# Performance work log

Measured on AMD Instinct MI355X. Metric: run time of the kernel, lower is better.

Reference implementation:

```python
import jax, jax.numpy as jnp
import numpy as np

IN_DIM = 1024
OUT_DIM = 1024
QK_DIM = OUT_DIM // 4  # 256


def setup_inputs() -> dict:
    key = jax.random.key(0)
    kx, ky, kq, kk, kv = jax.random.split(key, 5)
    B, Sq, Sk = 16, 2048, 2048
    x = jax.random.normal(kx, (B, Sq, IN_DIM), dtype=jnp.float32)
    y = jax.random.normal(ky, (B, Sk, IN_DIM), dtype=jnp.float32)
    s = 1.0 / np.sqrt(IN_DIM)
    Wq = jax.random.normal(kq, (IN_DIM, QK_DIM), dtype=jnp.float32) * s
    Wk = jax.random.normal(kk, (IN_DIM, QK_DIM), dtype=jnp.float32) * s
    Wv = jax.random.normal(kv, (IN_DIM, OUT_DIM), dtype=jnp.float32) * s
    return {"x": x, "y": y, "Wq": Wq, "Wk": Wk, "Wv": Wv}


def reference(x, y, Wq, Wk, Wv):
    # q: [B,Sq,dk], k: [B,Sk,dk]
    q = jnp.einsum("bsd,dk->bsk", x, Wq)
    k = jnp.einsum("btd,dk->btk", y, Wk)
    # NOTE: original scales by out_dim**0.5, not qk dim
    scores = jnp.einsum("bsk,btk->bst", q, k) / jnp.sqrt(jnp.float32(OUT_DIM))
    attn = jax.nn.softmax(scores, axis=-1)
    v = jnp.einsum("btd,de->bte", y, Wv)
    out = jnp.einsum("bst,bte->bse", attn, v)
    return out + x
```

## Files before the change

kernel.cpp:

```cpp
#include <hip/hip_runtime.h>

typedef __attribute__((ext_vector_type(8))) short bf16x8;
typedef __attribute__((ext_vector_type(4))) short s16x4;
typedef __attribute__((ext_vector_type(4))) float f32x4;

#define MFMA16(a,b,c) __builtin_amdgcn_mfma_f32_16x16x32_bf16((a),(b),(c),0,0,0)

__device__ __forceinline__ unsigned short f2bf(float f) {
  unsigned int u = __float_as_uint(f);
  return (unsigned short)((u + 0x7fffu + ((u >> 16) & 1u)) >> 16);
}
__device__ __forceinline__ float bf2f(unsigned short u) {
  return __uint_as_float(((unsigned int)u) << 16);
}

__device__ __forceinline__ void gload16(const void* g, void* l) {
  __builtin_amdgcn_global_load_lds((const __attribute__((address_space(1))) void*)g,
                                   (__attribute__((address_space(3))) void*)l, 16, 0, 0);
}

__global__ __launch_bounds__(256) void cvt_bf16(const float* __restrict__ in,
                                                unsigned short* __restrict__ out, int n8) {
  for (int i = blockIdx.x * 256 + threadIdx.x; i < n8; i += gridDim.x * 256) {
    float4 a = ((const float4*)in)[2 * i];
    float4 b = ((const float4*)in)[2 * i + 1];
    s16x4 p0, p1;
    p0[0] = f2bf(a.x); p0[1] = f2bf(a.y); p0[2] = f2bf(a.z); p0[3] = f2bf(a.w);
    p1[0] = f2bf(b.x); p1[1] = f2bf(b.y); p1[2] = f2bf(b.z); p1[3] = f2bf(b.w);
    ((s16x4*)out)[2 * i] = p0;
    ((s16x4*)out)[2 * i + 1] = p1;
  }
}

__global__ __launch_bounds__(256) void tcvt(const float* __restrict__ W,
                                            unsigned short* __restrict__ Wt, int K, int N) {
  __shared__ float t[32][33];
  const int n0 = blockIdx.x * 32, k0 = blockIdx.y * 32;
  const int c = threadIdx.x & 31, r8 = threadIdx.x >> 5;
#pragma unroll
  for (int p = 0; p < 4; ++p) {
    int r = r8 + p * 8;
    t[r][c] = W[(size_t)(k0 + r) * N + n0 + c];
  }
  __syncthreads();
#pragma unroll
  for (int p = 0; p < 4; ++p) {
    int r = r8 + p * 8;
    Wt[(size_t)(n0 + r) * K + k0 + c] = f2bf(t[c][r]);
  }
}

__global__ __launch_bounds__(256) void proj_gemm(
    const unsigned short* __restrict__ A, const unsigned short* __restrict__ Bt,
    void* __restrict__ Cv, int N, int mode, float scale)
{
  __shared__ __align__(16) unsigned short As[2][4096];
  __shared__ __align__(16) unsigned short Bs[2][4096];
  const int tid = threadIdx.x, lane = tid & 63, w = tid >> 6;
  const int wr = w >> 1, wc = w & 1;
  const int lrow = lane & 15, lg = lane >> 4;
  const size_t bm = (size_t)blockIdx.x * 128;
  const size_t bn = (size_t)blockIdx.y * 128;
  const int rl = lane >> 2, cq = lane & 3;

  auto stage = [&](int kt, int buf) {
#pragma unroll
    for (int u = 0; u < 2; ++u) {
      int row = w * 32 + u * 16 + rl;
      gload16(A  + (bm + row) * 1024 + kt * 32 + cq * 8, &As[buf][(w * 32 + u * 16) * 32]);
      gload16(Bt + (bn + row) * 1024 + kt * 32 + cq * 8, &Bs[buf][(w * 32 + u * 16) * 32]);
    }
  };

  f32x4 acc[4][4] = {};
  stage(0, 0);
  __syncthreads();

  for (int kt = 0; kt < 32; ++kt) {
    const int cur = kt & 1;
    if (kt + 1 < 32) stage(kt + 1, cur ^ 1);
    bf16x8 af[4], bfr[4];
#pragma unroll
    for (int i = 0; i < 4; ++i)
      af[i] = *(const bf16x8*)&As[cur][(wr * 64 + i * 16 + lrow) * 32 + lg * 8];
#pragma unroll
    for (int j = 0; j < 4; ++j)
      bfr[j] = *(const bf16x8*)&Bs[cur][(wc * 64 + j * 16 + lrow) * 32 + lg * 8];
    __builtin_amdgcn_s_setprio(1);
#pragma unroll
    for (int i = 0; i < 4; ++i)
#pragma unroll
      for (int j = 0; j < 4; ++j)
        acc[i][j] = MFMA16(af[i], bfr[j], acc[i][j]);
    __builtin_amdgcn_s_setprio(0);
    __syncthreads();
  }

  const int orow0 = blockIdx.x * 128 + wr * 64;
  const int ocol0 = blockIdx.y * 128 + wc * 64;
  if (mode == 0) {
    unsigned short* C = (unsigned short*)Cv;
#pragma unroll
    for (int i = 0; i < 4; ++i)
#pragma unroll
      for (int j = 0; j < 4; ++j) {
        int col = ocol0 + j * 16 + lrow;
#pragma unroll
        for (int r = 0; r < 4; ++r) {
          int row = orow0 + i * 16 + lg * 4 + r;
          C[(size_t)row * N + col] = f2bf(acc[i][j][r] * scale);
        }
      }
  } else {
    unsigned char* C8 = (unsigned char*)Cv;
#pragma unroll
    for (int i = 0; i < 4; ++i) {
      int m0 = orow0 + i * 16 + lg * 4;
      int bb = m0 >> 11, t = m0 & 2047;
#pragma unroll
      for (int j = 0; j < 4; ++j) {
        int e = ocol0 + j * 16 + lrow;
        int pk = 0;
        pk = __builtin_amdgcn_cvt_pk_fp8_f32(acc[i][j][0], acc[i][j][1], pk, false);
        pk = __builtin_amdgcn_cvt_pk_fp8_f32(acc[i][j][2], acc[i][j][3], pk, true);
        *(unsigned int*)(C8 + (size_t)bb * 2097152 + (size_t)e * 2048 + t) = (unsigned int)pk;
      }
    }
  }
}

#define SBAR  do { __builtin_amdgcn_s_barrier(); __builtin_amdgcn_sched_barrier(0); } while (0)

template<int NT, int NTIL, int MODE>
__global__ __launch_bounds__(512) void gemm4p(
    const unsigned short* __restrict__ Aall, const unsigned short* __restrict__ Ball,
    size_t abatch, size_t bbatch, int lda, int ldb,
    unsigned short* __restrict__ Cb, const float* __restrict__ X,
    float* __restrict__ Out, int b0, int nb)
{
  __shared__ __align__(16) unsigned short lds[65536];
  const int bid = blockIdx.x;
  const int bloc = bid % nb, tl = bid / nb;
  const int mtile = tl / NTIL, ntile = tl % NTIL;
  const int gb = b0 + bloc;
  const unsigned short* Ag = Aall + (MODE == 0 ? (size_t)gb : (size_t)bloc) * abatch
                                  + (size_t)mtile * 256 * lda;
  const unsigned short* Bg = Ball + (size_t)gb * bbatch + (size_t)ntile * 256 * ldb;

  const int tid = threadIdx.x, lane = tid & 63, w = tid >> 6;
  const int wm = w >> 2, wn = w & 3;
  const int lrow = lane & 15, lg = lane >> 4;
  char* lb = (char*)lds;

  auto stageU = [&](const unsigned short* G, int ld, int kofs, int ubyte) {
#pragma unroll
    for (int i = 0; i < 2; ++i) {
      int c = tid + 512 * i;
      int row = c >> 2, q = c & 3;
      int qs = q ^ ((row >> 1) & 3);
      gload16(G + (size_t)row * ld + kofs + qs * 8, lb + ubyte + c * 16);
    }
  };
  auto rdfrag = [&](int ubyte, int row) -> bf16x8 {
    return *(const bf16x8*)(lb + ubyte + row * 64 + ((lg ^ ((row >> 1) & 3)) << 4));
  };

  f32x4 acc[8][4] = {};
  bf16x8 afA[4], afB[4], bfrA[4], bfrB[4];

  stageU(Ag, lda, 0,  (0 * 2 + 0) * 16384);
  stageU(Bg, ldb, 0,  (1 * 2 + 0) * 16384);
  stageU(Ag, lda, 32, (2 * 2 + 0) * 16384);
  stageU(Bg, ldb, 32, (3 * 2 + 0) * 16384);
  stageU(Ag, lda, 64, (0 * 2 + 1) * 16384);
  stageU(Bg, ldb, 64, (1 * 2 + 1) * 16384);
  asm volatile("s_waitcnt vmcnt(8)" ::: "memory");
  SBAR;
#pragma unroll
  for (int i = 0; i < 4; ++i) afA[i] = rdfrag(0, wm * 128 + i * 16 + lrow);
#pragma unroll
  for (int nf = 0; nf < 4; ++nf) bfrA[nf] = rdfrag(2 * 16384, wn * 64 + nf * 16 + lrow);

  for (int T = 0; T < NT; ++T) {
    const int pc = T & 1, pn = (T + 1) & 1;
    const int a1b = (2 * 2 + pc) * 16384, b1b = (3 * 2 + pc) * 16384;
    const int a0b = (0 * 2 + pc) * 16384, b0b = (1 * 2 + pc) * 16384;
    const int t1 = (T + 1 < NT) ? T + 1 : 0;
    const int t2 = (T + 2 < NT) ? T + 2 : 0;

#pragma unroll
    for (int i = 0; i < 4; ++i) afB[i] = rdfrag(a0b, wm * 128 + (i + 4) * 16 + lrow);
    stageU(Ag, lda, t1 * 64 + 32, (2 * 2 + pn) * 16384);
    asm volatile("s_waitcnt lgkmcnt(4)" ::: "memory");
    __builtin_amdgcn_sched_barrier(0);
    __builtin_amdgcn_s_setprio(1);
#pragma unroll
    for (int mf = 0; mf < 4; ++mf)
#pragma unroll
      for (int nf = 0; nf < 4; ++nf)
        acc[mf][nf] = MFMA16(afA[mf], bfrA[nf], acc[mf][nf]);
    __builtin_amdgcn_s_setprio(0);
    asm volatile("s_waitcnt vmcnt(6)" ::: "memory");
    SBAR;

#pragma unroll
    for (int i = 0; i < 4; ++i) afA[i] = rdfrag(a1b, wm * 128 + i * 16 + lrow);
#pragma unroll
    for (int nf = 0; nf < 4; ++nf) bfrB[nf] = rdfrag(b1b, wn * 64 + nf * 16 + lrow);
    stageU(Bg, ldb, t1 * 64 + 32, (3 * 2 + pn) * 16384);
    asm volatile("s_waitcnt lgkmcnt(8)" ::: "memory");
    __builtin_amdgcn_sched_barrier(0);
    __builtin_amdgcn_s_setprio(1);
#pragma unroll
    for (int mf = 0; mf < 4; ++mf)
#pragma unroll
      for (int nf = 0; nf < 4; ++nf)
        acc[mf + 4][nf] = MFMA16(afB[mf], bfrA[nf], acc[mf + 4][nf]);
    __builtin_amdgcn_s_setprio(0);
    SBAR;

#pragma unroll
    for (int i = 0; i < 4; ++i) afB[i] = rdfrag(a1b, wm * 128 + (i + 4) * 16 + lrow);
    stageU(Ag, lda, t2 * 64, (0 * 2 + pc) * 16384);
    asm volatile("s_waitcnt lgkmcnt(4)" ::: "memory");
    __builtin_amdgcn_sched_barrier(0);
    __builtin_amdgcn_s_setprio(1);
#pragma unroll
    for (int mf = 0; mf < 4; ++mf)
#pragma unroll
      for (int nf = 0; nf < 4; ++nf)
        acc[mf][nf] = MFMA16(afA[mf], bfrB[nf], acc[mf][nf]);
    __builtin_amdgcn_s_setprio(0);
    asm volatile("s_waitcnt vmcnt(6)" ::: "memory");
    SBAR;

#pragma unroll
    for (int i = 0; i < 4; ++i) afA[i] = rdfrag((0 * 2 + pn) * 16384, wm * 128 + i * 16 + lrow);
#pragma unroll
    for (int nf = 0; nf < 4; ++nf) bfrA[nf] = rdfrag((1 * 2 + pn) * 16384, wn * 64 + nf * 16 + lrow);
    stageU(Bg, ldb, t2 * 64, (1 * 2 + pc) * 16384);
    asm volatile("s_waitcnt lgkmcnt(8)" ::: "memory");
    __builtin_amdgcn_sched_barrier(0);
    __builtin_amdgcn_s_setprio(1);
#pragma unroll
    for (int mf = 0; mf < 4; ++mf)
#pragma unroll
      for (int nf = 0; nf < 4; ++nf)
        acc[mf + 4][nf] = MFMA16(afB[mf], bfrB[nf], acc[mf + 4][nf]);
    __builtin_amdgcn_s_setprio(0);
    SBAR;
  }

  {
    unsigned short* Cp = Cb + (size_t)bloc * 2048 * 2048;
#pragma unroll
    for (int mf = 0; mf < 8; ++mf)
#pragma unroll
      for (int r = 0; r < 4; ++r) {
        int row = mtile * 256 + wm * 128 + mf * 16 + lg * 4 + r;
#pragma unroll
        for (int nf = 0; nf < 4; ++nf) {
          int col = ntile * 256 + wn * 64 + nf * 16 + lrow;
          Cp[(size_t)row * 2048 + col] = f2bf(acc[mf][nf][r]);
        }
      }
  }
  (void)X; (void)Out;
}

__global__ __launch_bounds__(256) void softmax_kernel(
    const unsigned short* __restrict__ Sp, unsigned char* __restrict__ Pp) {
  const int row = blockIdx.x * 4 + (threadIdx.x >> 6);
  const int lane = threadIdx.x & 63;
  const unsigned short* rp = Sp + (size_t)row * 2048;
  bf16x8 raw[4];
#pragma unroll
  for (int c = 0; c < 4; ++c) raw[c] = *(const bf16x8*)(rp + c * 512 + lane * 8);
  float v[32];
#pragma unroll
  for (int c = 0; c < 4; ++c)
#pragma unroll
    for (int j = 0; j < 8; ++j) v[c * 8 + j] = bf2f((unsigned short)raw[c][j]);
  float mx = v[0];
#pragma unroll
  for (int j = 1; j < 32; ++j) mx = fmaxf(mx, v[j]);
  mx = fmaxf(mx, __shfl_xor(mx, 1));
  mx = fmaxf(mx, __shfl_xor(mx, 2));
  mx = fmaxf(mx, __shfl_xor(mx, 4));
  mx = fmaxf(mx, __shfl_xor(mx, 8));
  mx = fmaxf(mx, __shfl_xor(mx, 16));
  mx = fmaxf(mx, __shfl_xor(mx, 32));
  float sum = 0.f;
#pragma unroll
  for (int j = 0; j < 32; ++j) { v[j] = __expf(v[j] - mx); sum += v[j]; }
  sum += __shfl_xor(sum, 1);
  sum += __shfl_xor(sum, 2);
  sum += __shfl_xor(sum, 4);
  sum += __shfl_xor(sum, 8);
  sum += __shfl_xor(sum, 16);
  sum += __shfl_xor(sum, 32);
  const float scale = 64.0f / sum;
  unsigned char* rp8 = Pp + (size_t)row * 2048;
#pragma unroll
  for (int c = 0; c < 4; ++c) {
    int lo = 0, hi = 0;
    lo = __builtin_amdgcn_cvt_pk_fp8_f32(v[c * 8 + 0] * scale, v[c * 8 + 1] * scale, lo, false);
    lo = __builtin_amdgcn_cvt_pk_fp8_f32(v[c * 8 + 2] * scale, v[c * 8 + 3] * scale, lo, true);
    hi = __builtin_amdgcn_cvt_pk_fp8_f32(v[c * 8 + 4] * scale, v[c * 8 + 5] * scale, hi, false);
    hi = __builtin_amdgcn_cvt_pk_fp8_f32(v[c * 8 + 6] * scale, v[c * 8 + 7] * scale, hi, true);
    uint2 o; o.x = (unsigned int)lo; o.y = (unsigned int)hi;
    *(uint2*)(rp8 + c * 512 + lane * 8) = o;
  }
}

__global__ __launch_bounds__(512) void pvf8_kernel(
    const unsigned char* __restrict__ Pp,
    const unsigned char* __restrict__ Vt,
    const float* __restrict__ X, float* __restrict__ Out,
    int b0, int nb)
{
  __shared__ __align__(16) unsigned char lds[4][32768];
  const int bloc = blockIdx.x % nb, tl = blockIdx.x / nb;
  const int mtile = tl >> 2, ntile = tl & 3;
  const int gb = b0 + bloc;
  const unsigned char* Ag = Pp + (size_t)bloc * 4194304 + (size_t)mtile * 256 * 2048;
  const unsigned char* Bg = Vt + (size_t)gb * 2097152 + (size_t)ntile * 256 * 2048;
  const int NT = 32;
  const int tid = threadIdx.x, lane = tid & 63, w = tid >> 6;
  const int wm = w >> 2, wn = w & 3;
  const int lrow = lane & 15, lg = lane >> 4;

  auto stageT = [&](int jt, int slot) {
#pragma unroll
    for (int i = 0; i < 2; ++i) {
      int c = tid + 512 * i; int row = c >> 2; int q = (c & 3) ^ ((row >> 1) & 3);
      gload16(Ag + (size_t)row * 2048 + jt * 64 + q * 16, &lds[slot][c * 16]);
    }
#pragma unroll
    for (int i = 0; i < 2; ++i) {
      int c = tid + 512 * i; int row = c >> 2; int q = (c & 3) ^ ((row >> 1) & 3);
      gload16(Bg + (size_t)row * 2048 + jt * 64 + q * 16, &lds[slot][16384 + c * 16]);
    }
  };

  f32x4 acc[8][4] = {};
  stageT(0, 0); stageT(1, 1); stageT(2, 2);

  for (int jt = 0; jt < NT; ++jt) {
    if (jt < NT - 2)       asm volatile("s_waitcnt vmcnt(8)" ::: "memory");
    else if (jt == NT - 2) asm volatile("s_waitcnt vmcnt(4)" ::: "memory");
    else                   asm volatile("s_waitcnt vmcnt(0)" ::: "memory");
    __builtin_amdgcn_sched_barrier(0);
    __builtin_amdgcn_s_barrier();
    __builtin_amdgcn_sched_barrier(0);
    if (jt + 3 < NT) stageT(jt + 3, (jt + 3) & 3);
    const int slot = jt & 3;
    long2 av[8], bv[4];
#pragma unroll
    for (int mf = 0; mf < 8; ++mf) {
      int row = wm * 128 + mf * 16 + lrow;
      av[mf] = *(const long2*)&lds[slot][row * 64 + ((lg ^ ((row >> 1) & 3)) << 4)];
    }
#pragma unroll
    for (int nf = 0; nf < 4; ++nf) {
      int row = wn * 64 + nf * 16 + lrow;
      bv[nf] = *(const long2*)&lds[slot][16384 + row * 64 + ((lg ^ ((row >> 1) & 3)) << 4)];
    }
    __builtin_amdgcn_s_setprio(1);
#pragma unroll
    for (int mf = 0; mf < 8; ++mf)
#pragma unroll
      for (int nf = 0; nf < 4; ++nf) {
        acc[mf][nf] = __builtin_amdgcn_mfma_f32_16x16x32_fp8_fp8(av[mf].x, bv[nf].x, acc[mf][nf], 0, 0, 0);
        acc[mf][nf] = __builtin_amdgcn_mfma_f32_16x16x32_fp8_fp8(av[mf].y, bv[nf].y, acc[mf][nf], 0, 0, 0);
      }
    __builtin_amdgcn_s_setprio(0);
  }

#pragma unroll
  for (int mf = 0; mf < 8; ++mf)
#pragma unroll
    for (int r = 0; r < 4; ++r) {
      int row = mtile * 256 + wm * 128 + mf * 16 + lg * 4 + r;
      const float* xr = X   + ((size_t)gb * 2048 + row) * 1024;
      float*      orp = Out + ((size_t)gb * 2048 + row) * 1024;
#pragma unroll
      for (int nf = 0; nf < 4; ++nf) {
        int col = ntile * 256 + wn * 64 + nf * 16 + lrow;
        orp[col] = acc[mf][nf][r] * 0.015625f + xr[col];
      }
    }
}

extern "C" void kernel_launch(void* const* d_in, const int* in_sizes, int n_in,
                              void* d_out, int out_size, void* d_ws, size_t ws_size,
                              hipStream_t stream) {
  (void)in_sizes; (void)n_in; (void)out_size;
  const float* x  = (const float*)d_in[0];
  const float* y  = (const float*)d_in[1];
  const float* Wq = (const float*)d_in[2];
  const float* Wk = (const float*)d_in[3];
  const float* Wv = (const float*)d_in[4];
  float* out = (float*)d_out;

  unsigned short* xb = (unsigned short*)d_out;
  unsigned short* yb = xb + (size_t)16 * 2048 * 1024;

  char* p = (char*)d_ws;
  unsigned short* Wqt = (unsigned short*)p;  p += (size_t)256 * 1024 * 2;
  unsigned short* Wkt = (unsigned short*)p;  p += (size_t)256 * 1024 * 2;
  unsigned short* Wvt = (unsigned short*)p;  p += (size_t)1024 * 1024 * 2;
  unsigned short* qws = (unsigned short*)p;  p += (size_t)16 * 2048 * 256 * 2;
  unsigned short* kws = (unsigned short*)p;  p += (size_t)16 * 2048 * 256 * 2;
  unsigned char*  vt8 = (unsigned char*)p;   p += (size_t)16 * 1024 * 2048;
  char* dyn = p;
  const size_t fixed_bytes = (size_t)(dyn - (char*)d_ws);
  const size_t per_batch = (size_t)2048 * 2048 * 2 + (size_t)2048 * 2048;
  int nb = 1;
  if      (ws_size >= fixed_bytes + 16 * per_batch) nb = 16;
  else if (ws_size >= fixed_bytes + 8  * per_batch) nb = 8;
  else if (ws_size >= fixed_bytes + 4  * per_batch) nb = 4;
  else if (ws_size >= fixed_bytes + 2  * per_batch) nb = 2;
  else nb = 1;
  unsigned short* Sp = (unsigned short*)dyn;
  unsigned char*  Pp = (unsigned char*)(dyn + (size_t)nb * 2048 * 2048 * 2);

  const int n8 = (16 * 2048 * 1024) / 8;
  cvt_bf16<<<2048, 256, 0, stream>>>(x, xb, n8);
  cvt_bf16<<<2048, 256, 0, stream>>>(y, yb, n8);
  tcvt<<<dim3(8, 32),  256, 0, stream>>>(Wq, Wqt, 1024, 256);
  tcvt<<<dim3(8, 32),  256, 0, stream>>>(Wk, Wkt, 1024, 256);
  tcvt<<<dim3(32, 32), 256, 0, stream>>>(Wv, Wvt, 1024, 1024);

  proj_gemm<<<dim3(256, 2), 256, 0, stream>>>(xb, Wqt, (void*)qws, 256, 0, 0.03125f);
  proj_gemm<<<dim3(256, 2), 256, 0, stream>>>(yb, Wkt, (void*)kws, 256, 0, 1.0f);
  proj_gemm<<<dim3(256, 8), 256, 0, stream>>>(yb, Wvt, (void*)vt8, 1024, 2, 1.0f);

  for (int b0 = 0; b0 < 16; b0 += nb) {
    gemm4p<4, 8, 0><<<nb * 64, 512, 0, stream>>>(
        qws, kws, (size_t)2048 * 256, (size_t)2048 * 256, 256, 256,
        Sp, nullptr, nullptr, b0, nb);
    softmax_kernel<<<nb * 512, 256, 0, stream>>>(Sp, Pp);
    pvf8_kernel<<<nb * 32, 512, 0, stream>>>(Pp, vt8, x, out, b0, nb);
  }
}
```

Measured before the change: 510.8 us.

## Pre-pack V into MFMA fragment layout and load B operands directly from global

The V projection epilogue now writes fp8 V in a blocked layout where each 16-column by 64-token group is a contiguous 1 KB fragment. The PV kernel then loads its B fragments straight from global memory into registers instead of staging them through LDS. The output tile is halved to 256x128, which doubles the grid, halves LDS use, and drops the accumulators to 8x2. The intent is less LDS traffic and more occupancy and parallelism, at the cost of unhidden global-load latency on V and more redundant reads of the P tile across blocks.

```diff
diff --git a/kernel.cpp b/kernel.cpp
--- a/kernel.cpp
+++ b/kernel.cpp
@@ -117,13 +117,17 @@
     for (int i = 0; i < 4; ++i) {
       int m0 = orow0 + i * 16 + lg * 4;
       int bb = m0 >> 11, t = m0 & 2047;
+      int tw = t >> 6, t64 = t & 63;
 #pragma unroll
       for (int j = 0; j < 4; ++j) {
         int e = ocol0 + j * 16 + lrow;
+        int eg = e >> 4;
         int pk = 0;
         pk = __builtin_amdgcn_cvt_pk_fp8_f32(acc[i][j][0], acc[i][j][1], pk, false);
         pk = __builtin_amdgcn_cvt_pk_fp8_f32(acc[i][j][2], acc[i][j][3], pk, true);
-        *(unsigned int*)(C8 + (size_t)bb * 2097152 + (size_t)e * 2048 + t) = (unsigned int)pk;
+        *(unsigned int*)(C8 + (size_t)bb * 2097152
+                            + ((size_t)(eg * 32 + tw)) * 1024 + lrow * 64 + t64)
+            = (unsigned int)pk;
       }
     }
   }
@@ -184,7 +188,7 @@
   for (int T = 0; T < NT; ++T) {
     const int pc = T & 1, pn = (T + 1) & 1;
     const int a1b = (2 * 2 + pc) * 16384, b1b = (3 * 2 + pc) * 16384;
-    const int a0b = (0 * 2 + pc) * 16384, b0b = (1 * 2 + pc) * 16384;
+    const int a0b = (0 * 2 + pc) * 16384;
     const int t1 = (T + 1 < NT) ? T + 1 : 0;
     const int t2 = (T + 2 < NT) ? T + 2 : 0;
 
@@ -315,66 +319,78 @@
 
 __global__ __launch_bounds__(512) void pvf8_kernel(
     const unsigned char* __restrict__ Pp,
-    const unsigned char* __restrict__ Vt,
+    const unsigned char* __restrict__ Vp,
     const float* __restrict__ X, float* __restrict__ Out,
     int b0, int nb)
 {
-  __shared__ __align__(16) unsigned char lds[4][32768];
+  __shared__ __align__(16) unsigned char lds[4][16384];
   const int bloc = blockIdx.x % nb, tl = blockIdx.x / nb;
-  const int mtile = tl >> 2, ntile = tl & 3;
+  const int mtile = tl >> 3, ntile = tl & 7;
   const int gb = b0 + bloc;
   const unsigned char* Ag = Pp + (size_t)bloc * 4194304 + (size_t)mtile * 256 * 2048;
-  const unsigned char* Bg = Vt + (size_t)gb * 2097152 + (size_t)ntile * 256 * 2048;
+  const unsigned char* Vb = Vp + (size_t)gb * 2097152;
   const int NT = 32;
   const int tid = threadIdx.x, lane = tid & 63, w = tid >> 6;
   const int wm = w >> 2, wn = w & 3;
   const int lrow = lane & 15, lg = lane >> 4;
 
-  auto stageT = [&](int jt, int slot) {
+  auto stageA = [&](int jt) {
+    unsigned char* dst = lds[jt & 3];
 #pragma unroll
     for (int i = 0; i < 2; ++i) {
       int c = tid + 512 * i; int row = c >> 2; int q = (c & 3) ^ ((row >> 1) & 3);
-      gload16(Ag + (size_t)row * 2048 + jt * 64 + q * 16, &lds[slot][c * 16]);
-    }
-#pragma unroll
-    for (int i = 0; i < 2; ++i) {
-      int c = tid + 512 * i; int row = c >> 2; int q = (c & 3) ^ ((row >> 1) & 3);
-      gload16(Bg + (size_t)row * 2048 + jt * 64 + q * 16, &lds[slot][16384 + c * 16]);
+      gload16(Ag + (size_t)row * 2048 + jt * 64 + q * 16, dst + c * 16);
     }
   };
 
-  f32x4 acc[8][4] = {};
-  stageT(0, 0); stageT(1, 1); stageT(2, 2);
+  f32x4 acc[8][2] = {};
+  stageA(0); stageA(1); stageA(2);
+  asm volatile("s_waitcnt vmcnt(4)" ::: "memory");
 
   for (int jt = 0; jt < NT; ++jt) {
-    if (jt < NT - 2)       asm volatile("s_waitcnt vmcnt(8)" ::: "memory");
-    else if (jt == NT - 2) asm volatile("s_waitcnt vmcnt(4)" ::: "memory");
-    else                   asm volatile("s_waitcnt vmcnt(0)" ::: "memory");
-    __builtin_amdgcn_sched_barrier(0);
     __builtin_amdgcn_s_barrier();
-    __builtin_amdgcn_sched_barrier(0);
-    if (jt + 3 < NT) stageT(jt + 3, (jt + 3) & 3);
-    const int slot = jt & 3;
-    long2 av[8], bv[4];
-#pragma unroll
-    for (int mf = 0; mf < 8; ++mf) {
-      int row = wm * 128 + mf * 16 + lrow;
-      av[mf] = *(const long2*)&lds[slot][row * 64 + ((lg ^ ((row >> 1) & 3)) << 4)];
-    }
-#pragma unroll
-    for (int nf = 0; nf < 4; ++nf) {
-      int row = wn * 64 + nf * 16 + lrow;
-      bv[nf] = *(const long2*)&lds[slot][16384 + row * 64 + ((lg ^ ((row >> 1) & 3)) << 4)];
-    }
-    __builtin_amdgcn_s_setprio(1);
-#pragma unroll
-    for (int mf = 0; mf < 8; ++mf)
-#pragma unroll
-      for (int nf = 0; nf < 4; ++nf) {
-        acc[mf][nf] = __builtin_amdgcn_mfma_f32_16x16x32_fp8_fp8(av[mf].x, bv[nf].x, acc[mf][nf], 0, 0, 0);
-        acc[mf][nf] = __builtin_amdgcn_mfma_f32_16x16x32_fp8_fp8(av[mf].y, bv[nf].y, acc[mf][nf], 0, 0, 0);
-      }
-    __builtin_amdgcn_s_setprio(0);
+    long2 bv[2];
+#pragma unroll
+    for (int nf = 0; nf < 2; ++nf) {
+      int eg = ntile * 8 + wn * 2 + nf;
+      bv[nf] = *(const long2*)(Vb + ((size_t)(eg * 32 + jt)) * 1024 + lrow * 64 + lg * 16);
+    }
+    if (jt + 3 < NT) stageA(jt + 3);
+    const unsigned char* Ab = lds[jt & 3];
+    {
+      long2 av[4];
+#pragma unroll
+      for (int mf = 0; mf < 4; ++mf) {
+        int row = wm * 128 + mf * 16 + lrow;
+        av[mf] = *(const long2*)(Ab + row * 64 + ((lg ^ ((row >> 1) & 3)) << 4));
+      }
+      __builtin_amdgcn_s_setprio(1);
+#pragma unroll
+      for (int mf = 0; mf < 4; ++mf)
+#pragma unroll
+        for (int nf = 0; nf < 2; ++nf) {
+          acc[mf][nf] = __builtin_amdgcn_mfma_f32_16x16x32_fp8_fp8(av[mf].x, bv[nf].x, acc[mf][nf], 0, 0, 0);
+          acc[mf][nf] = __builtin_amdgcn_mfma_f32_16x16x32_fp8_fp8(av[mf].y, bv[nf].y, acc[mf][nf], 0, 0, 0);
+        }
+      __builtin_amdgcn_s_setprio(0);
+    }
+    {
+      long2 av[4];
+#pragma unroll
+      for (int mf = 0; mf < 4; ++mf) {
+        int row = wm * 128 + (mf + 4) * 16 + lrow;
+        av[mf] = *(const long2*)(Ab + row * 64 + ((lg ^ ((row >> 1) & 3)) << 4));
+      }
+      __builtin_amdgcn_s_setprio(1);
+#pragma unroll
+      for (int mf = 0; mf < 4; ++mf)
+#pragma unroll
+        for (int nf = 0; nf < 2; ++nf) {
+          acc[mf + 4][nf] = __builtin_amdgcn_mfma_f32_16x16x32_fp8_fp8(av[mf].x, bv[nf].x, acc[mf + 4][nf], 0, 0, 0);
+          acc[mf + 4][nf] = __builtin_amdgcn_mfma_f32_16x16x32_fp8_fp8(av[mf].y, bv[nf].y, acc[mf + 4][nf], 0, 0, 0);
+        }
+      __builtin_amdgcn_s_setprio(0);
+    }
   }
 
 #pragma unroll
@@ -385,8 +401,8 @@
       const float* xr = X   + ((size_t)gb * 2048 + row) * 1024;
       float*      orp = Out + ((size_t)gb * 2048 + row) * 1024;
 #pragma unroll
-      for (int nf = 0; nf < 4; ++nf) {
-        int col = ntile * 256 + wn * 64 + nf * 16 + lrow;
+      for (int nf = 0; nf < 2; ++nf) {
+        int col = ntile * 128 + wn * 32 + nf * 16 + lrow;
         orp[col] = acc[mf][nf][r] * 0.015625f + xr[col];
       }
     }
@@ -412,7 +428,7 @@
   unsigned short* Wvt = (unsigned short*)p;  p += (size_t)1024 * 1024 * 2;
   unsigned short* qws = (unsigned short*)p;  p += (size_t)16 * 2048 * 256 * 2;
   unsigned short* kws = (unsigned short*)p;  p += (size_t)16 * 2048 * 256 * 2;
-  unsigned char*  vt8 = (unsigned char*)p;   p += (size_t)16 * 1024 * 2048;
+  unsigned char*  vp8 = (unsigned char*)p;   p += (size_t)16 * 1024 * 2048;
   char* dyn = p;
   const size_t fixed_bytes = (size_t)(dyn - (char*)d_ws);
   const size_t per_batch = (size_t)2048 * 2048 * 2 + (size_t)2048 * 2048;
@@ -434,13 +450,13 @@
 
   proj_gemm<<<dim3(256, 2), 256, 0, stream>>>(xb, Wqt, (void*)qws, 256, 0, 0.03125f);
   proj_gemm<<<dim3(256, 2), 256, 0, stream>>>(yb, Wkt, (void*)kws, 256, 0, 1.0f);
-  proj_gemm<<<dim3(256, 8), 256, 0, stream>>>(yb, Wvt, (void*)vt8, 1024, 2, 1.0f);
+  proj_gemm<<<dim3(256, 8), 256, 0, stream>>>(yb, Wvt, (void*)vp8, 1024, 2, 1.0f);
 
   for (int b0 = 0; b0 < 16; b0 += nb) {
     gemm4p<4, 8, 0><<<nb * 64, 512, 0, stream>>>(
         qws, kws, (size_t)2048 * 256, (size_t)2048 * 256, 256, 256,
         Sp, nullptr, nullptr, b0, nb);
     softmax_kernel<<<nb * 512, 256, 0, stream>>>(Sp, Pp);
-    pvf8_kernel<<<nb * 32, 512, 0, stream>>>(Pp, vt8, x, out, b0, nb);
-  }
-}
+    pvf8_kernel<<<nb * 64, 512, 0, stream>>>(Pp, vp8, x, out, b0, nb);
+  }
+}
```

New measurement: 494.9 us. -3.1%, faster.
